# Optimization experiments

Measured on AMD Instinct MI355X. Metric: run time of the kernel, lower is better.

The kernel has to match this reference:

```python
import jax, jax.numpy as jnp
import numpy as np

HID, H, D = 128, 4, 32
NB, NP, NC = 60000, 2000, 4000
EM, EP, EI = 150000, 300000, 150000


def segment_softmax(logits, seg, n):
    # logits: [E, H], seg: [E] destination ids
    m = jax.ops.segment_max(logits, seg, num_segments=n)
    m = jnp.where(jnp.isfinite(m), m, 0.0)  # guard empty segments
    e = jnp.exp(logits - m[seg])
    s = jax.ops.segment_sum(e, seg, num_segments=n)
    return e / (s[seg] + 1e-16)


def layer_norm(x, g, b):
    mu = x.mean(-1, keepdims=True)
    v = ((x - mu) ** 2).mean(-1, keepdims=True)
    return (x - mu) / jnp.sqrt(v + 1e-5) * g + b


def setup_inputs():
    key = jax.random.key(0)
    ks = jax.random.split(key, 40)
    i = iter(range(40))
    nrm = lambda shape, s=1.0: jax.random.normal(ks[next(i)], shape, jnp.float32) * s
    w = lambda shape: nrm(shape, 0.05)
    inp = {
        'x_ball': nrm((NB, HID)),
        'x_player': nrm((NP, HID)),
        'x_context': nrm((NC, HID)),
        'em': jnp.stack([jax.random.randint(ks[next(i)], (EM,), 0, NP),
                         jax.random.randint(ks[next(i)], (EM,), 0, NB)]),
        'ep': jnp.stack([jax.random.randint(ks[next(i)], (EP,), 0, NB),
                         jax.random.randint(ks[next(i)], (EP,), 0, NB)]),
        'ei': jnp.stack([jax.random.randint(ks[next(i)], (EI,), 0, NB),
                         jax.random.randint(ks[next(i)], (EI,), 0, NC)]),
        'ea_p': nrm((EP, 1)),
        # GATv2Conv (player -matchup-> ball)
        'g_Wl': w((HID, HID)), 'g_Wr': w((HID, HID)), 'g_att': w((H, D)), 'g_b': jnp.zeros((HID,), jnp.float32),
        # TransformerConv (ball -recent_precedes-> ball), edge_dim=1
        't_Wq': w((HID, HID)), 't_bq': jnp.zeros((HID,), jnp.float32),
        't_Wk': w((HID, HID)), 't_bk': jnp.zeros((HID,), jnp.float32),
        't_Wv': w((HID, HID)), 't_bv': jnp.zeros((HID,), jnp.float32),
        't_We': w((1, HID)),
        't_Wskip': w((HID, HID)), 't_bskip': jnp.zeros((HID,), jnp.float32),
        # SAGEConv mean (ball -informs-> context)
        's_Wl': w((HID, HID)), 's_bl': jnp.zeros((HID,), jnp.float32), 's_Wr': w((HID, HID)),
        # per-type LayerNorms (only applied to types produced by the conv)
        'ln_ball_g': jnp.ones((HID,), jnp.float32), 'ln_ball_b': jnp.zeros((HID,), jnp.float32),
        'ln_ctx_g': jnp.ones((HID,), jnp.float32), 'ln_ctx_b': jnp.zeros((HID,), jnp.float32),
    }
    return inp


def reference(x_ball, x_player, x_context, em, ep, ei, ea_p,
              g_Wl, g_Wr, g_att, g_b,
              t_Wq, t_bq, t_Wk, t_bk, t_Wv, t_bv, t_We, t_Wskip, t_bskip,
              s_Wl, s_bl, s_Wr,
              ln_ball_g, ln_ball_b, ln_ctx_g, ln_ctx_b):
    # ---- GATv2Conv: player -> ball ----
    src, dst = em[0], em[1]
    xl = (x_player @ g_Wl).reshape(NP, H, D)   # src transform
    xr = (x_ball @ g_Wr).reshape(NB, H, D)     # dst transform
    e = xl[src] + xr[dst]                      # [EM, H, D]
    e = jnp.where(e > 0, e, 0.2 * e)           # leaky_relu(0.2)
    logit = jnp.einsum('ehd,hd->eh', e, g_att)
    alpha = segment_softmax(logit, dst, NB)
    gat = jax.ops.segment_sum(xl[src] * alpha[..., None], dst, num_segments=NB)
    gat = gat.reshape(NB, HID) + g_b

    # ---- TransformerConv: ball -> ball, edge_dim=1 ----
    src, dst = ep[0], ep[1]
    q = (x_ball @ t_Wq + t_bq).reshape(NB, H, D)
    k = (x_ball @ t_Wk + t_bk).reshape(NB, H, D)
    v = (x_ball @ t_Wv + t_bv).reshape(NB, H, D)
    ee = (ea_p @ t_We).reshape(EP, H, D)       # lin_edge (no bias)
    kj = k[src] + ee
    logit = jnp.einsum('ehd,ehd->eh', q[dst], kj) / jnp.sqrt(jnp.float32(D))
    alpha = segment_softmax(logit, dst, NB)
    tr = jax.ops.segment_sum((v[src] + ee) * alpha[..., None], dst, num_segments=NB)
    tr = tr.reshape(NB, HID) + x_ball @ t_Wskip + t_bskip  # root/skip connection

    # ---- SAGEConv mean: ball -> context ----
    src, dst = ei[0], ei[1]
    summ = jax.ops.segment_sum(x_ball[src], dst, num_segments=NC)
    cnt = jax.ops.segment_sum(jnp.ones((EI,), jnp.float32), dst, num_segments=NC)
    mean = summ / jnp.maximum(cnt, 1.0)[:, None]
    sage = mean @ s_Wl + s_bl + x_context @ s_Wr

    # ---- HeteroConv aggr='sum' + residual + per-type LayerNorm ----
    ball_out = layer_norm(gat + tr + x_ball, ln_ball_g, ln_ball_b)
    ctx_out = layer_norm(sage + x_context, ln_ctx_g, ln_ctx_b)
    # 'player' receives no messages -> passed through unchanged
    return (ball_out, ctx_out, x_player)
```

## Files before the change

kernel.cpp:

```cpp
#include <hip/hip_runtime.h>
#include <hip/hip_bf16.h>

#define NB 60000
#define NP 2000
#define NC 4000
#define EM_N 150000
#define EP_N 300000
#define EI_N 150000
#define POOL_N (EM_N + EP_N + EI_N)
#define SEG_TOT (NB + NB + NC)
#define SCAN_BLK 1024
#define NPART ((SEG_TOT + SCAN_BLK - 1) / SCAN_BLK)
#define BALL_BLKS ((NB + 127) / 128)
#define PLYR_BLKS ((NP + 127) / 128)
#define CTXG_BLKS ((NC + 127) / 128)
#define GEMM_BLKS (BALL_BLKS + PLYR_BLKS + CTXG_BLKS)
#define FILL_BLKS ((POOL_N + 255) / 256)
#define COPY_BLKS ((NP * 128 + 255) / 256)
#define BBALL ((NB + 3) / 4)

typedef __hip_bfloat16 bf16;
typedef unsigned int u32;
typedef __attribute__((ext_vector_type(8))) short s8v;
typedef __attribute__((ext_vector_type(4))) float f4v;

__device__ __forceinline__ short f2bs(float f) {
    bf16 h = __float2bfloat16(f);
    return __builtin_bit_cast(short, h);
}
__device__ __forceinline__ float bsToF(short s) {
    return __builtin_bit_cast(float, ((unsigned)(unsigned short)s) << 16);
}
__device__ __forceinline__ float loF(u32 v) { return bsToF((short)(v & 0xffff)); }
__device__ __forceinline__ float hiF(u32 v) { return bsToF((short)(v >> 16)); }
__device__ __forceinline__ u32 packbf(float a, float b) {
    return (u32)(unsigned short)f2bs(a) | ((u32)(unsigned short)f2bs(b) << 16);
}

__global__ void hist_wt_copy_kernel(const int* __restrict__ em, const int* __restrict__ ep,
                                    const int* __restrict__ ei, int* __restrict__ counts,
                                    const float* __restrict__ W0, const float* __restrict__ W1,
                                    const float* __restrict__ W2, const float* __restrict__ W3,
                                    const float* __restrict__ W4, const float* __restrict__ W5,
                                    const float* __restrict__ W6, const float* __restrict__ W7,
                                    ushort* __restrict__ Wt,
                                    const float* __restrict__ x_player, float* __restrict__ out) {
    if (blockIdx.x >= FILL_BLKS) {
        int t = (blockIdx.x - FILL_BLKS) * 256 + threadIdx.x;
        if (t < NP * 128) out[(size_t)(NB + NC) * 128 + t] = x_player[t];
        return;
    }
    int t = blockIdx.x * 256 + threadIdx.x;
    if (t < 8 * 16384) {
        int w = t >> 14, r = t & 16383, k = r >> 7, n = r & 127;
        const float* W = (w == 0) ? W0 : (w == 1) ? W1 : (w == 2) ? W2 : (w == 3) ? W3
                       : (w == 4) ? W4 : (w == 5) ? W5 : (w == 6) ? W6 : W7;
        int sc = (n >> 5) * 32 + ((n & 1) << 4) + ((n & 31) >> 1);
        Wt[w * 16384 + sc * 128 + k] = (unsigned short)f2bs(W[k * 128 + n]);
    }
    if (t < EM_N) atomicAdd(&counts[em[EM_N + t]], 1);
    else if (t < EM_N + EP_N) atomicAdd(&counts[NB + ep[EP_N + (t - EM_N)]], 1);
    else if (t < POOL_N) atomicAdd(&counts[2 * NB + ei[EI_N + (t - EM_N - EP_N)]], 1);
}

__global__ void scan_fused_kernel(const int* __restrict__ counts, int* __restrict__ offsets,
                                  int* __restrict__ cursors, int* __restrict__ gbase) {
    __shared__ int sd[256];
    __shared__ int sbase;
    int b = blockIdx.x, tid = threadIdx.x;
    int base = b * SCAN_BLK + tid * 4;
    int v[4]; int ts = 0;
#pragma unroll
    for (int j = 0; j < 4; j++) { int idx = base + j; v[j] = (idx < SEG_TOT) ? counts[idx] : 0; ts += v[j]; }
    sd[tid] = ts;
    for (int off = 1; off < 256; off <<= 1) {
        __syncthreads(); int t = (tid >= off) ? sd[tid - off] : 0;
        __syncthreads(); sd[tid] += t;
    }
    __syncthreads();
    if (tid == 255) sbase = atomicAdd(gbase, sd[255]);
    __syncthreads();
    int run = sd[tid] - ts + sbase;
#pragma unroll
    for (int j = 0; j < 4; j++) {
        int idx = base + j;
        if (idx < SEG_TOT) { offsets[idx] = run; cursors[idx] = run; }
        run += v[j];
    }
}

__device__ __forceinline__ void mfma_pass(const s8v a[2][4], const ushort* __restrict__ wt,
                                          const float* __restrict__ bp, const float* __restrict__ Ares,
                                          int mbase, int M, int l16, int quad,
                                          u32* __restrict__ op, int stride) {
#pragma unroll
    for (int t = 0; t < 4; t++) {
        s8v blo[4], bhi[4];
#pragma unroll
        for (int kt = 0; kt < 4; kt++) {
            blo[kt] = *(const s8v*)(wt + (t * 32 + l16) * 128 + kt * 32 + quad * 8);
            bhi[kt] = *(const s8v*)(wt + (t * 32 + 16 + l16) * 128 + kt * 32 + quad * 8);
        }
        float bvlo = 0.f, bvhi = 0.f;
        if (bp) { float2 b2 = ((const float2*)bp)[t * 16 + l16]; bvlo = b2.x; bvhi = b2.y; }
#pragma unroll
        for (int mt = 0; mt < 2; mt++) {
            f4v alo = {0.f, 0.f, 0.f, 0.f}, ahi = {0.f, 0.f, 0.f, 0.f};
#pragma unroll
            for (int kt = 0; kt < 4; kt++) {
                alo = __builtin_amdgcn_mfma_f32_16x16x32_bf16(a[mt][kt], blo[kt], alo, 0, 0, 0);
                ahi = __builtin_amdgcn_mfma_f32_16x16x32_bf16(a[mt][kt], bhi[kt], ahi, 0, 0, 0);
            }
#pragma unroll
            for (int r = 0; r < 4; r++) {
                int row = mbase + mt * 16 + quad * 4 + r;
                if (row < M) {
                    float vlo = alo[r] + bvlo, vhi = ahi[r] + bvhi;
                    if (Ares) {
                        float2 xr2 = ((const float2*)Ares)[(size_t)row * 64 + t * 16 + l16];
                        vlo += xr2.x; vhi += xr2.y;
                    }
                    op[(size_t)row * stride + t * 16 + l16] = packbf(vlo, vhi);
                }
            }
        }
    }
}

__global__ __launch_bounds__(256) void gemm6_fill_kernel(
    const float* __restrict__ Aball, const float* __restrict__ Aplyr, const float* __restrict__ Actx,
    const ushort* __restrict__ Wt,
    const float* __restrict__ bq, const float* __restrict__ bk,
    const float* __restrict__ bv_, const float* __restrict__ bskip,
    const float* __restrict__ g_b, const float* __restrict__ bl,
    u32* __restrict__ xrP, u32* __restrict__ qP, uint2* __restrict__ kvP,
    u32* __restrict__ skipP, u32* __restrict__ xlP, u32* __restrict__ xwP,
    u32* __restrict__ ctxlinP,
    const int* __restrict__ em, const int* __restrict__ ep, const int* __restrict__ ei,
    const float* __restrict__ ea_p, int* __restrict__ cursors, int2* __restrict__ pool) {
    if (blockIdx.x >= GEMM_BLKS) {
        int t = (blockIdx.x - GEMM_BLKS) * 256 + threadIdx.x;
        int seg, s; float ea = 0.f;
        if (t < EM_N) { s = em[t]; seg = em[EM_N + t]; }
        else if (t < EM_N + EP_N) { int e = t - EM_N; s = ep[e]; seg = NB + ep[EP_N + e]; ea = ea_p[e]; }
        else if (t < POOL_N) { int e = t - EM_N - EP_N; s = ei[e]; seg = 2 * NB + ei[EI_N + e]; }
        else return;
        int pos = atomicAdd(&cursors[seg], 1);
        pool[pos] = make_int2(s, __float_as_int(ea));
        return;
    }
    const int lane = threadIdx.x & 63;
    const int wv = threadIdx.x >> 6;
    const int quad = lane >> 4, l16 = lane & 15;
    int kind, bidx;
    if (blockIdx.x < BALL_BLKS) { kind = 0; bidx = blockIdx.x; }
    else if (blockIdx.x < BALL_BLKS + PLYR_BLKS) { kind = 1; bidx = blockIdx.x - BALL_BLKS; }
    else { kind = 2; bidx = blockIdx.x - BALL_BLKS - PLYR_BLKS; }
    const int M = (kind == 0) ? NB : (kind == 1) ? NP : NC;
    const float* A = (kind == 0) ? Aball : (kind == 1) ? Aplyr : Actx;
    const int mbase = bidx * 128 + wv * 32;

    s8v a[2][4];
#pragma unroll
    for (int mt = 0; mt < 2; mt++) {
        int row = mbase + mt * 16 + l16;
        if (row >= M) row = M - 1;
        const float* ap = A + (size_t)row * 128 + quad * 8;
#pragma unroll
        for (int kt = 0; kt < 4; kt++) {
            const float4* p = (const float4*)(ap + kt * 32);
            float4 u = p[0], v = p[1];
            s8v f;
            f[0] = f2bs(u.x); f[1] = f2bs(u.y); f[2] = f2bs(u.z); f[3] = f2bs(u.w);
            f[4] = f2bs(v.x); f[5] = f2bs(v.y); f[6] = f2bs(v.z); f[7] = f2bs(v.w);
            a[mt][kt] = f;
        }
    }

    if (kind == 1) {
        mfma_pass(a, Wt + 5 * 16384, nullptr, nullptr, mbase, M, l16, quad, xlP, 64);
        return;
    }
    if (kind == 2) {
        mfma_pass(a, Wt + 7 * 16384, bl, Actx, mbase, M, l16, quad, ctxlinP, 64);
        return;
    }
    mfma_pass(a, Wt + 0 * 16384, nullptr, nullptr, mbase, M, l16, quad, xrP, 64);
    mfma_pass(a, Wt + 1 * 16384, bq, nullptr, mbase, M, l16, quad, qP, 64);
    {
        const ushort* wtk = Wt + 2 * 16384;
        const ushort* wtv = Wt + 3 * 16384;
#pragma unroll
        for (int t = 0; t < 4; t++) {
            float2 bk2 = ((const float2*)bk)[t * 16 + l16];
            float2 bv2 = ((const float2*)bv_)[t * 16 + l16];
            u32 kpk[2][4];
            {
                s8v blo[4], bhi[4];
#pragma unroll
                for (int kt = 0; kt < 4; kt++) {
                    blo[kt] = *(const s8v*)(wtk + (t * 32 + l16) * 128 + kt * 32 + quad * 8);
                    bhi[kt] = *(const s8v*)(wtk + (t * 32 + 16 + l16) * 128 + kt * 32 + quad * 8);
                }
#pragma unroll
                for (int mt = 0; mt < 2; mt++) {
                    f4v alo = {0.f, 0.f, 0.f, 0.f}, ahi = {0.f, 0.f, 0.f, 0.f};
#pragma unroll
                    for (int kt = 0; kt < 4; kt++) {
                        alo = __builtin_amdgcn_mfma_f32_16x16x32_bf16(a[mt][kt], blo[kt], alo, 0, 0, 0);
                        ahi = __builtin_amdgcn_mfma_f32_16x16x32_bf16(a[mt][kt], bhi[kt], ahi, 0, 0, 0);
                    }
#pragma unroll
                    for (int r = 0; r < 4; r++)
                        kpk[mt][r] = packbf(alo[r] + bk2.x, ahi[r] + bk2.y);
                }
            }
            {
                s8v blo[4], bhi[4];
#pragma unroll
                for (int kt = 0; kt < 4; kt++) {
                    blo[kt] = *(const s8v*)(wtv + (t * 32 + l16) * 128 + kt * 32 + quad * 8);
                    bhi[kt] = *(const s8v*)(wtv + (t * 32 + 16 + l16) * 128 + kt * 32 + quad * 8);
                }
#pragma unroll
                for (int mt = 0; mt < 2; mt++) {
                    f4v alo = {0.f, 0.f, 0.f, 0.f}, ahi = {0.f, 0.f, 0.f, 0.f};
#pragma unroll
                    for (int kt = 0; kt < 4; kt++) {
                        alo = __builtin_amdgcn_mfma_f32_16x16x32_bf16(a[mt][kt], blo[kt], alo, 0, 0, 0);
                        ahi = __builtin_amdgcn_mfma_f32_16x16x32_bf16(a[mt][kt], bhi[kt], ahi, 0, 0, 0);
                    }
#pragma unroll
                    for (int r = 0; r < 4; r++) {
                        int row = mbase + mt * 16 + quad * 4 + r;
                        if (row < NB)
                            kvP[(size_t)row * 64 + t * 16 + l16] =
                                make_uint2(kpk[mt][r], packbf(alo[r] + bv2.x, ahi[r] + bv2.y));
                    }
                }
            }
        }
    }
    mfma_pass(a, Wt + 4 * 16384, bskip, Aball, mbase, M, l16, quad, skipP, 64);
    mfma_pass(a, Wt + 6 * 16384, nullptr, nullptr, mbase, M, l16, quad, xwP, 64);
}


__global__ __launch_bounds__(256) void ball_sage_kernel(
    const u32* __restrict__ xlP, const u32* __restrict__ xrP, const u32* __restrict__ qP,
    const uint2* __restrict__ kvP, const u32* __restrict__ skipP, const u32* __restrict__ xwP,
    const u32* __restrict__ ctxlinP,
    const float* __restrict__ g_att, const float* __restrict__ g_b, const float* __restrict__ We,
    const int* __restrict__ offsets, const int* __restrict__ counts,
    const int2* __restrict__ pool,
    const float* __restrict__ ln_g, const float* __restrict__ ln_b,
    const float* __restrict__ cg, const float* __restrict__ cb,
    float* __restrict__ out) {
    __shared__ float part[4][128];
    const int wv = threadIdx.x >> 6, l = threadIdx.x & 63;

    if (blockIdx.x >= BBALL) {
        int c = blockIdx.x - BBALL;
        int beg = offsets[2 * NB + c], cnt = counts[2 * NB + c];
        float s0 = 0.f, s1 = 0.f;
        for (int j = wv; j < cnt; j += 4) {
            u32 xv = xwP[(size_t)pool[beg + j].x * 64 + l];
            s0 += loF(xv); s1 += hiF(xv);
        }
        part[wv][l * 2] = s0; part[wv][l * 2 + 1] = s1;
        __syncthreads();
        if (wv == 0) {
            float m = fmaxf((float)cnt, 1.f);
            u32 cl = ctxlinP[(size_t)c * 64 + l];
            float v0 = (part[0][l * 2] + part[1][l * 2] + part[2][l * 2] + part[3][l * 2]) / m + loF(cl);
            float v1 = (part[0][l * 2 + 1] + part[1][l * 2 + 1] + part[2][l * 2 + 1] + part[3][l * 2 + 1]) / m + hiF(cl);
            float s = v0 + v1;
#pragma unroll
            for (int m2 = 1; m2 <= 32; m2 <<= 1) s += __shfl_xor(s, m2);
            float mu = s * (1.f / 128.f);
            float d0 = v0 - mu, d1 = v1 - mu;
            float qv = d0 * d0 + d1 * d1;
#pragma unroll
            for (int m2 = 1; m2 <= 32; m2 <<= 1) qv += __shfl_xor(qv, m2);
            float inv = rsqrtf(qv * (1.f / 128.f) + 1e-5f);
            float2 g2 = ((const float2*)cg)[l];
            float2 b2 = ((const float2*)cb)[l];
            ((float2*)out)[(size_t)(NB + c) * 64 + l] =
                make_float2(d0 * inv * g2.x + b2.x, d1 * inv * g2.y + b2.y);
        }
        return;
    }

    const int d = blockIdx.x * 4 + wv;
    const size_t rowD = (size_t)d * 64;

    float2 att = ((const float2*)g_att)[l];
    u32 xr2 = xrP[rowD + l];
    float xr0 = loF(xr2), xr1 = hiF(xr2);
    int beg = offsets[d], cnt = counts[d];
    float n0 = 0.f, n1 = 0.f, deg = 0.f;
    for (int j = 0; j < cnt; j += 4) {
        int sI[4]; bool ok[4];
#pragma unroll
        for (int i = 0; i < 4; i++) {
            ok[i] = (j + i < cnt);
            sI[i] = ok[i] ? pool[beg + j + i].x : 0;
        }
        u32 xv[4];
#pragma unroll
        for (int i = 0; i < 4; i++) xv[i] = xlP[(size_t)sI[i] * 64 + l];
        float p[4], xa[4], xb[4];
#pragma unroll
        for (int i = 0; i < 4; i++) {
            xa[i] = loF(xv[i]); xb[i] = hiF(xv[i]);
            float u0 = xa[i] + xr0; u0 = u0 > 0.f ? u0 : 0.2f * u0;
            float u1 = xb[i] + xr1; u1 = u1 > 0.f ? u1 : 0.2f * u1;
            p[i] = u0 * att.x + u1 * att.y;
        }
#pragma unroll
        for (int m = 1; m <= 8; m <<= 1) {
#pragma unroll
            for (int i = 0; i < 4; i++) p[i] += __shfl_xor(p[i], m);
        }
#pragma unroll
        for (int i = 0; i < 4; i++) {
            p[i] = ok[i] ? __expf(p[i]) : 0.f;
            n0 += p[i] * xa[i]; n1 += p[i] * xb[i]; deg += p[i];
        }
    }
    float gat0 = n0 / (deg + 1e-16f), gat1 = n1 / (deg + 1e-16f);

    u32 q2 = qP[rowD + l];
    float q0 = loF(q2), q1 = hiF(q2);
    float2 we = ((const float2*)We)[l];
    float dw = q0 * we.x + q1 * we.y;
#pragma unroll
    for (int m = 1; m <= 8; m <<= 1) dw += __shfl_xor(dw, m);
    beg = offsets[NB + d]; cnt = counts[NB + d];
    float sv0 = 0.f, sv1 = 0.f, spe = 0.f, det = 0.f;
    for (int j = 0; j < cnt; j += 4) {
        int2 pr[4]; bool ok[4];
#pragma unroll
        for (int i = 0; i < 4; i++) {
            ok[i] = (j + i < cnt);
            pr[i] = ok[i] ? pool[beg + j + i] : make_int2(0, 0);
        }
        uint2 kv[4];
#pragma unroll
        for (int i = 0; i < 4; i++) kv[i] = kvP[(size_t)pr[i].x * 64 + l];
        float p[4], ea[4];
#pragma unroll
        for (int i = 0; i < 4; i++) {
            ea[i] = __int_as_float(pr[i].y);
            p[i] = q0 * loF(kv[i].x) + q1 * hiF(kv[i].x);
        }
#pragma unroll
        for (int m = 1; m <= 8; m <<= 1) {
#pragma unroll
            for (int i = 0; i < 4; i++) p[i] += __shfl_xor(p[i], m);
        }
#pragma unroll
        for (int i = 0; i < 4; i++) {
            p[i] = ok[i] ? __expf((p[i] + ea[i] * dw) * 0.17677669529663687f) : 0.f;
            sv0 += p[i] * loF(kv[i].y); sv1 += p[i] * hiF(kv[i].y);
            spe += p[i] * ea[i]; det += p[i];
        }
    }
    float tr0 = (sv0 + spe * we.x) / (det + 1e-16f);
    float tr1 = (sv1 + spe * we.y) / (det + 1e-16f);

    u32 sk = skipP[rowD + l];
    float2 gb2 = ((const float2*)g_b)[l];
    float val0 = loF(sk) + gb2.x + gat0 + tr0;
    float val1 = hiF(sk) + gb2.y + gat1 + tr1;
    float s = val0 + val1;
#pragma unroll
    for (int m = 1; m <= 32; m <<= 1) s += __shfl_xor(s, m);
    float mu = s * (1.f / 128.f);
    float d0 = val0 - mu, d1 = val1 - mu;
    float qv = d0 * d0 + d1 * d1;
#pragma unroll
    for (int m = 1; m <= 32; m <<= 1) qv += __shfl_xor(qv, m);
    float inv = rsqrtf(qv * (1.f / 128.f) + 1e-5f);
    float2 g2 = ((const float2*)ln_g)[l];
    float2 b2 = ((const float2*)ln_b)[l];
    ((float2*)out)[rowD + l] = make_float2(d0 * inv * g2.x + b2.x, d1 * inv * g2.y + b2.y);
}

extern "C" void kernel_launch(void* const* d_in, const int* in_sizes, int n_in,
                              void* d_out, int out_size, void* d_ws, size_t ws_size,
                              hipStream_t stream) {
    const float* x_ball = (const float*)d_in[0];
    const float* x_player = (const float*)d_in[1];
    const float* x_context = (const float*)d_in[2];
    const int* em = (const int*)d_in[3];
    const int* ep = (const int*)d_in[4];
    const int* ei = (const int*)d_in[5];
    const float* ea_p = (const float*)d_in[6];
    const float* g_Wl = (const float*)d_in[7];
    const float* g_Wr = (const float*)d_in[8];
    const float* g_att = (const float*)d_in[9];
    const float* g_b = (const float*)d_in[10];
    const float* t_Wq = (const float*)d_in[11];
    const float* t_bq = (const float*)d_in[12];
    const float* t_Wk = (const float*)d_in[13];
    const float* t_bk = (const float*)d_in[14];
    const float* t_Wv = (const float*)d_in[15];
    const float* t_bv = (const float*)d_in[16];
    const float* t_We = (const float*)d_in[17];
    const float* t_Wskip = (const float*)d_in[18];
    const float* t_bskip = (const float*)d_in[19];
    const float* s_Wl = (const float*)d_in[20];
    const float* s_bl = (const float*)d_in[21];
    const float* s_Wr = (const float*)d_in[22];
    const float* ln_ball_g = (const float*)d_in[23];
    const float* ln_ball_b = (const float*)d_in[24];
    const float* ln_ctx_g = (const float*)d_in[25];
    const float* ln_ctx_b = (const float*)d_in[26];
    float* out = (float*)d_out;

    float* ws = (float*)d_ws;
    size_t o = 0;
    int* counts = (int*)(ws + o);   o += SEG_TOT;
    int* gbase = (int*)(ws + o);    o += 1;
    int* offsets = (int*)(ws + o);  o += SEG_TOT;
    int* cursors = (int*)(ws + o);  o += SEG_TOT;
    if (o & 1) o++;
    int2* pool = (int2*)(ws + o);   o += (size_t)POOL_N * 2;
    ushort* Wt = (ushort*)(ws + o); o += (8 * 16384) / 2;
    u32* xlP = (u32*)(ws + o);      o += (size_t)NP * 64;
    u32* xrP = (u32*)(ws + o);      o += (size_t)NB * 64;
    u32* qP = (u32*)(ws + o);       o += (size_t)NB * 64;
    u32* skipP = (u32*)(ws + o);    o += (size_t)NB * 64;
    u32* xwP = (u32*)(ws + o);      o += (size_t)NB * 64;
    u32* ctxlinP = (u32*)(ws + o);  o += (size_t)NC * 64;
    if (o & 1) o++;
    uint2* kvP = (uint2*)(ws + o);  o += (size_t)NB * 128;

    dim3 blk(256);
    hipMemsetAsync(counts, 0, (SEG_TOT + 1) * sizeof(int), stream);
    hist_wt_copy_kernel<<<FILL_BLKS + COPY_BLKS, blk, 0, stream>>>(
        em, ep, ei, counts, g_Wr, t_Wq, t_Wk, t_Wv, t_Wskip, g_Wl, s_Wl, s_Wr, Wt, x_player, out);
    scan_fused_kernel<<<NPART, blk, 0, stream>>>(counts, offsets, cursors, gbase);
    gemm6_fill_kernel<<<GEMM_BLKS + FILL_BLKS, blk, 0, stream>>>(
        x_ball, x_player, x_context, Wt, t_bq, t_bk, t_bv, t_bskip, g_b, s_bl,
        xrP, qP, kvP, skipP, xlP, xwP, ctxlinP, em, ep, ei, ea_p, cursors, pool);
    ball_sage_kernel<<<BBALL + NC, blk, 0, stream>>>(
        xlP, xrP, qP, kvP, skipP, xwP, ctxlinP, g_att, g_b, t_We,
        offsets, counts, pool, ln_ball_g, ln_ball_b, ln_ctx_g, ln_ctx_b, out);
}
```

Measured before the change: 327.6 us.

## Stage weight tiles into LDS via direct global-to-LDS loads in GEMM kernel

The fused GEMM kernel now copies each 128x128 bf16 weight matrix into shared memory with global_load_lds before computing, instead of having every wave read B fragments straight from global memory. The weight layout is changed to a k-chunked arrangement that suits the LDS reads, and the workspace pointer is aligned to 16 bytes for the direct loads. Rows per block drop from 128 to 64 (16 per wave), which doubles the block count. The trade is more syncthreads and staging rounds per block, and less register reuse of B across row tiles.

```diff
diff --git a/kernel.cpp b/kernel.cpp
--- a/kernel.cpp
+++ b/kernel.cpp
@@ -11,9 +11,9 @@
 #define SEG_TOT (NB + NB + NC)
 #define SCAN_BLK 1024
 #define NPART ((SEG_TOT + SCAN_BLK - 1) / SCAN_BLK)
-#define BALL_BLKS ((NB + 127) / 128)
-#define PLYR_BLKS ((NP + 127) / 128)
-#define CTXG_BLKS ((NC + 127) / 128)
+#define BALL_BLKS ((NB + 63) / 64)
+#define PLYR_BLKS ((NP + 63) / 64)
+#define CTXG_BLKS ((NC + 63) / 64)
 #define GEMM_BLKS (BALL_BLKS + PLYR_BLKS + CTXG_BLKS)
 #define FILL_BLKS ((POOL_N + 255) / 256)
 #define COPY_BLKS ((NP * 128 + 255) / 256)
@@ -35,6 +35,10 @@
 __device__ __forceinline__ float hiF(u32 v) { return bsToF((short)(v >> 16)); }
 __device__ __forceinline__ u32 packbf(float a, float b) {
     return (u32)(unsigned short)f2bs(a) | ((u32)(unsigned short)f2bs(b) << 16);
+}
+__device__ __forceinline__ void gl_lds16(const void* g, void* l) {
+    __builtin_amdgcn_global_load_lds((const __attribute__((address_space(1))) void*)g,
+                                     (__attribute__((address_space(3))) void*)l, 16, 0, 0);
 }
 
 __global__ void hist_wt_copy_kernel(const int* __restrict__ em, const int* __restrict__ ep,
@@ -56,7 +60,7 @@
         const float* W = (w == 0) ? W0 : (w == 1) ? W1 : (w == 2) ? W2 : (w == 3) ? W3
                        : (w == 4) ? W4 : (w == 5) ? W5 : (w == 6) ? W6 : W7;
         int sc = (n >> 5) * 32 + ((n & 1) << 4) + ((n & 31) >> 1);
-        Wt[w * 16384 + sc * 128 + k] = (unsigned short)f2bs(W[k * 128 + n]);
+        Wt[w * 16384 + (k >> 3) * 1024 + sc * 8 + (k & 7)] = (unsigned short)f2bs(W[k * 128 + n]);
     }
     if (t < EM_N) atomicAdd(&counts[em[EM_N + t]], 1);
     else if (t < EM_N + EP_N) atomicAdd(&counts[NB + ep[EP_N + (t - EM_N)]], 1);
@@ -89,39 +93,33 @@
     }
 }
 
-__device__ __forceinline__ void mfma_pass(const s8v a[2][4], const ushort* __restrict__ wt,
-                                          const float* __restrict__ bp, const float* __restrict__ Ares,
-                                          int mbase, int M, int l16, int quad,
-                                          u32* __restrict__ op, int stride) {
+__device__ __forceinline__ void pass_compute(const ushort* __restrict__ lds, const s8v a[4],
+                                             const float* __restrict__ bp,
+                                             const float* __restrict__ Ares,
+                                             int mbase, int M, int l16, int quad,
+                                             u32* __restrict__ op) {
 #pragma unroll
     for (int t = 0; t < 4; t++) {
-        s8v blo[4], bhi[4];
+        f4v alo = {0.f, 0.f, 0.f, 0.f}, ahi = {0.f, 0.f, 0.f, 0.f};
 #pragma unroll
         for (int kt = 0; kt < 4; kt++) {
-            blo[kt] = *(const s8v*)(wt + (t * 32 + l16) * 128 + kt * 32 + quad * 8);
-            bhi[kt] = *(const s8v*)(wt + (t * 32 + 16 + l16) * 128 + kt * 32 + quad * 8);
+            s8v blo = *(const s8v*)(lds + (kt * 4 + quad) * 1024 + (t * 32 + l16) * 8);
+            s8v bhi = *(const s8v*)(lds + (kt * 4 + quad) * 1024 + (t * 32 + 16 + l16) * 8);
+            alo = __builtin_amdgcn_mfma_f32_16x16x32_bf16(a[kt], blo, alo, 0, 0, 0);
+            ahi = __builtin_amdgcn_mfma_f32_16x16x32_bf16(a[kt], bhi, ahi, 0, 0, 0);
         }
         float bvlo = 0.f, bvhi = 0.f;
         if (bp) { float2 b2 = ((const float2*)bp)[t * 16 + l16]; bvlo = b2.x; bvhi = b2.y; }
 #pragma unroll
-        for (int mt = 0; mt < 2; mt++) {
-            f4v alo = {0.f, 0.f, 0.f, 0.f}, ahi = {0.f, 0.f, 0.f, 0.f};
-#pragma unroll
-            for (int kt = 0; kt < 4; kt++) {
-                alo = __builtin_amdgcn_mfma_f32_16x16x32_bf16(a[mt][kt], blo[kt], alo, 0, 0, 0);
-                ahi = __builtin_amdgcn_mfma_f32_16x16x32_bf16(a[mt][kt], bhi[kt], ahi, 0, 0, 0);
-            }
-#pragma unroll
-            for (int r = 0; r < 4; r++) {
-                int row = mbase + mt * 16 + quad * 4 + r;
-                if (row < M) {
-                    float vlo = alo[r] + bvlo, vhi = ahi[r] + bvhi;
-                    if (Ares) {
-                        float2 xr2 = ((const float2*)Ares)[(size_t)row * 64 + t * 16 + l16];
-                        vlo += xr2.x; vhi += xr2.y;
-                    }
-                    op[(size_t)row * stride + t * 16 + l16] = packbf(vlo, vhi);
+        for (int r = 0; r < 4; r++) {
+            int row = mbase + quad * 4 + r;
+            if (row < M) {
+                float vlo = alo[r] + bvlo, vhi = ahi[r] + bvhi;
+                if (Ares) {
+                    float2 xr2 = ((const float2*)Ares)[(size_t)row * 64 + t * 16 + l16];
+                    vlo += xr2.x; vhi += xr2.y;
                 }
+                op[(size_t)row * 64 + t * 16 + l16] = packbf(vlo, vhi);
             }
         }
     }
@@ -138,6 +136,7 @@
     u32* __restrict__ ctxlinP,
     const int* __restrict__ em, const int* __restrict__ ep, const int* __restrict__ ei,
     const float* __restrict__ ea_p, int* __restrict__ cursors, int2* __restrict__ pool) {
+    __shared__ ushort lds[16384];
     if (blockIdx.x >= GEMM_BLKS) {
         int t = (blockIdx.x - GEMM_BLKS) * 256 + threadIdx.x;
         int seg, s; float ea = 0.f;
@@ -149,8 +148,9 @@
         pool[pos] = make_int2(s, __float_as_int(ea));
         return;
     }
-    const int lane = threadIdx.x & 63;
-    const int wv = threadIdx.x >> 6;
+    const int tid = threadIdx.x;
+    const int lane = tid & 63;
+    const int wv = tid >> 6;
     const int quad = lane >> 4, l16 = lane & 15;
     int kind, bidx;
     if (blockIdx.x < BALL_BLKS) { kind = 0; bidx = blockIdx.x; }
@@ -158,12 +158,21 @@
     else { kind = 2; bidx = blockIdx.x - BALL_BLKS - PLYR_BLKS; }
     const int M = (kind == 0) ? NB : (kind == 1) ? NP : NC;
     const float* A = (kind == 0) ? Aball : (kind == 1) ? Aplyr : Actx;
-    const int mbase = bidx * 128 + wv * 32;
-
-    s8v a[2][4];
-#pragma unroll
-    for (int mt = 0; mt < 2; mt++) {
-        int row = mbase + mt * 16 + l16;
+    const int mbase = bidx * 64 + wv * 16;
+    const int ldsbase = wv * 512;
+
+#define STAGE(W) do { \
+    const ushort* _src = Wt + (W) * 16384; \
+    _Pragma("unroll") \
+    for (int p = 0; p < 8; p++) \
+        gl_lds16(_src + (size_t)(p * 256 + tid) * 8, lds + p * 2048 + ldsbase); \
+} while (0)
+
+    STAGE(kind == 0 ? 0 : (kind == 1 ? 5 : 7));
+
+    s8v a[4];
+    {
+        int row = mbase + l16;
         if (row >= M) row = M - 1;
         const float* ap = A + (size_t)row * 128 + quad * 8;
 #pragma unroll
@@ -173,78 +182,64 @@
             s8v f;
             f[0] = f2bs(u.x); f[1] = f2bs(u.y); f[2] = f2bs(u.z); f[3] = f2bs(u.w);
             f[4] = f2bs(v.x); f[5] = f2bs(v.y); f[6] = f2bs(v.z); f[7] = f2bs(v.w);
-            a[mt][kt] = f;
-        }
-    }
+            a[kt] = f;
+        }
+    }
+    __syncthreads();
 
     if (kind == 1) {
-        mfma_pass(a, Wt + 5 * 16384, nullptr, nullptr, mbase, M, l16, quad, xlP, 64);
+        pass_compute(lds, a, nullptr, nullptr, mbase, M, l16, quad, xlP);
         return;
     }
     if (kind == 2) {
-        mfma_pass(a, Wt + 7 * 16384, bl, Actx, mbase, M, l16, quad, ctxlinP, 64);
+        pass_compute(lds, a, bl, Actx, mbase, M, l16, quad, ctxlinP);
         return;
     }
-    mfma_pass(a, Wt + 0 * 16384, nullptr, nullptr, mbase, M, l16, quad, xrP, 64);
-    mfma_pass(a, Wt + 1 * 16384, bq, nullptr, mbase, M, l16, quad, qP, 64);
-    {
-        const ushort* wtk = Wt + 2 * 16384;
-        const ushort* wtv = Wt + 3 * 16384;
-#pragma unroll
-        for (int t = 0; t < 4; t++) {
-            float2 bk2 = ((const float2*)bk)[t * 16 + l16];
-            float2 bv2 = ((const float2*)bv_)[t * 16 + l16];
-            u32 kpk[2][4];
-            {
-                s8v blo[4], bhi[4];
-#pragma unroll
-                for (int kt = 0; kt < 4; kt++) {
-                    blo[kt] = *(const s8v*)(wtk + (t * 32 + l16) * 128 + kt * 32 + quad * 8);
-                    bhi[kt] = *(const s8v*)(wtk + (t * 32 + 16 + l16) * 128 + kt * 32 + quad * 8);
-                }
-#pragma unroll
-                for (int mt = 0; mt < 2; mt++) {
-                    f4v alo = {0.f, 0.f, 0.f, 0.f}, ahi = {0.f, 0.f, 0.f, 0.f};
-#pragma unroll
-                    for (int kt = 0; kt < 4; kt++) {
-                        alo = __builtin_amdgcn_mfma_f32_16x16x32_bf16(a[mt][kt], blo[kt], alo, 0, 0, 0);
-                        ahi = __builtin_amdgcn_mfma_f32_16x16x32_bf16(a[mt][kt], bhi[kt], ahi, 0, 0, 0);
-                    }
-#pragma unroll
-                    for (int r = 0; r < 4; r++)
-                        kpk[mt][r] = packbf(alo[r] + bk2.x, ahi[r] + bk2.y);
-                }
-            }
-            {
-                s8v blo[4], bhi[4];
-#pragma unroll
-                for (int kt = 0; kt < 4; kt++) {
-                    blo[kt] = *(const s8v*)(wtv + (t * 32 + l16) * 128 + kt * 32 + quad * 8);
-                    bhi[kt] = *(const s8v*)(wtv + (t * 32 + 16 + l16) * 128 + kt * 32 + quad * 8);
-                }
-#pragma unroll
-                for (int mt = 0; mt < 2; mt++) {
-                    f4v alo = {0.f, 0.f, 0.f, 0.f}, ahi = {0.f, 0.f, 0.f, 0.f};
-#pragma unroll
-                    for (int kt = 0; kt < 4; kt++) {
-                        alo = __builtin_amdgcn_mfma_f32_16x16x32_bf16(a[mt][kt], blo[kt], alo, 0, 0, 0);
-                        ahi = __builtin_amdgcn_mfma_f32_16x16x32_bf16(a[mt][kt], bhi[kt], ahi, 0, 0, 0);
-                    }
-#pragma unroll
-                    for (int r = 0; r < 4; r++) {
-                        int row = mbase + mt * 16 + quad * 4 + r;
-                        if (row < NB)
-                            kvP[(size_t)row * 64 + t * 16 + l16] =
-                                make_uint2(kpk[mt][r], packbf(alo[r] + bv2.x, ahi[r] + bv2.y));
-                    }
-                }
-            }
-        }
-    }
-    mfma_pass(a, Wt + 4 * 16384, bskip, Aball, mbase, M, l16, quad, skipP, 64);
-    mfma_pass(a, Wt + 6 * 16384, nullptr, nullptr, mbase, M, l16, quad, xwP, 64);
-}
-
+    pass_compute(lds, a, nullptr, nullptr, mbase, M, l16, quad, xrP);
+    __syncthreads(); STAGE(1); __syncthreads();
+    pass_compute(lds, a, bq, nullptr, mbase, M, l16, quad, qP);
+    __syncthreads(); STAGE(2); __syncthreads();
+    u32 kpk[4][4];
+#pragma unroll
+    for (int t = 0; t < 4; t++) {
+        f4v alo = {0.f, 0.f, 0.f, 0.f}, ahi = {0.f, 0.f, 0.f, 0.f};
+#pragma unroll
+        for (int kt = 0; kt < 4; kt++) {
+            s8v blo = *(const s8v*)(lds + (kt * 4 + quad) * 1024 + (t * 32 + l16) * 8);
+            s8v bhi = *(const s8v*)(lds + (kt * 4 + quad) * 1024 + (t * 32 + 16 + l16) * 8);
+            alo = __builtin_amdgcn_mfma_f32_16x16x32_bf16(a[kt], blo, alo, 0, 0, 0);
+            ahi = __builtin_amdgcn_mfma_f32_16x16x32_bf16(a[kt], bhi, ahi, 0, 0, 0);
+        }
+        float2 bk2 = ((const float2*)bk)[t * 16 + l16];
+#pragma unroll
+        for (int r = 0; r < 4; r++) kpk[t][r] = packbf(alo[r] + bk2.x, ahi[r] + bk2.y);
+    }
+    __syncthreads(); STAGE(3); __syncthreads();
+#pragma unroll
+    for (int t = 0; t < 4; t++) {
+        f4v alo = {0.f, 0.f, 0.f, 0.f}, ahi = {0.f, 0.f, 0.f, 0.f};
+#pragma unroll
+        for (int kt = 0; kt < 4; kt++) {
+            s8v blo = *(const s8v*)(lds + (kt * 4 + quad) * 1024 + (t * 32 + l16) * 8);
+            s8v bhi = *(const s8v*)(lds + (kt * 4 + quad) * 1024 + (t * 32 + 16 + l16) * 8);
+            alo = __builtin_amdgcn_mfma_f32_16x16x32_bf16(a[kt], blo, alo, 0, 0, 0);
+            ahi = __builtin_amdgcn_mfma_f32_16x16x32_bf16(a[kt], bhi, ahi, 0, 0, 0);
+        }
+        float2 bv2 = ((const float2*)bv_)[t * 16 + l16];
+#pragma unroll
+        for (int r = 0; r < 4; r++) {
+            int row = mbase + quad * 4 + r;
+            if (row < NB)
+                kvP[(size_t)row * 64 + t * 16 + l16] =
+                    make_uint2(kpk[t][r], packbf(alo[r] + bv2.x, ahi[r] + bv2.y));
+        }
+    }
+    __syncthreads(); STAGE(4); __syncthreads();
+    pass_compute(lds, a, bskip, Aball, mbase, M, l16, quad, skipP);
+    __syncthreads(); STAGE(6); __syncthreads();
+    pass_compute(lds, a, nullptr, nullptr, mbase, M, l16, quad, xwP);
+#undef STAGE
+}
 
 __global__ __launch_bounds__(256) void ball_sage_kernel(
     const u32* __restrict__ xlP, const u32* __restrict__ xrP, const u32* __restrict__ qP,
@@ -427,6 +422,7 @@
     int* cursors = (int*)(ws + o);  o += SEG_TOT;
     if (o & 1) o++;
     int2* pool = (int2*)(ws + o);   o += (size_t)POOL_N * 2;
+    o = (o + 3) & ~(size_t)3;
     ushort* Wt = (ushort*)(ws + o); o += (8 * 16384) / 2;
     u32* xlP = (u32*)(ws + o);      o += (size_t)NP * 64;
     u32* xrP = (u32*)(ws + o);      o += (size_t)NB * 64;
```

After: 305.3 us. -6.8%, faster.
